# Performance work log

Hardware: AMD Instinct MI355X
Metric: run time of the kernel (lower is better)

## Reference

```python
import jax, jax.numpy as jnp
import numpy as np

EPS = 1e-8  # torch F.cosine_similarity eps


def setup_inputs() -> dict:
    key = jax.random.key(0)
    k1, k2, k3 = jax.random.split(key, 3)
    bn, cn, dim = 4096, 8192, 1024
    x = jax.random.normal(k1, (bn, dim), dtype=jnp.float32)
    positive = jax.random.normal(k2, (bn, dim), dtype=jnp.float32)
    negative = jax.random.normal(k3, (cn, dim), dtype=jnp.float32)
    return {"x": x, "positive": positive, "negative": negative}


def reference(x, positive, negative):
    bn = x.shape[0]
    nx = jnp.linalg.norm(x, axis=1)          # (bn,)
    npos = jnp.linalg.norm(positive, axis=1)  # (bn,)
    nneg = jnp.linalg.norm(negative, axis=1)  # (cn,)
    # positive cosine similarity, torch-style eps clamp on norm product
    sim = jnp.sum(x * positive, axis=1) / jnp.maximum(nx * npos, EPS)  # (bn,)
    # negative cosine similarities via one matmul instead of (bn,cn,dim) repeats
    neg_sim = (x @ negative.T) / jnp.maximum(nx[:, None] * nneg[None, :], EPS)  # (bn,cn)
    p = jnp.exp(sim) / jnp.sum(jnp.exp(neg_sim), axis=1)  # (bn,)
    loss = -jnp.sum(jnp.log(p)) / bn
    return loss
```

## Files before the change

### kernel.cpp

```cpp
#include <hip/hip_runtime.h>
#include <stdint.h>
#include <stddef.h>

#define DIM 1024
#define EPS 1e-8f

typedef __attribute__((ext_vector_type(4))) float f32x4;
typedef __attribute__((ext_vector_type(2))) long longx2;

__device__ __forceinline__ void async_copy16(const void* g, void* l) {
    __builtin_amdgcn_global_load_lds(
        (__attribute__((address_space(1))) void*)const_cast<void*>(g),
        (__attribute__((address_space(3))) void*)(l), 16, 0, 0);
}

#define PIPE_SYNC(N) asm volatile("s_waitcnt vmcnt(" #N ")\n\ts_barrier" ::: "memory")

__global__ __launch_bounds__(256)
void prep_all(const float* __restrict__ x, const float* __restrict__ pos,
              const float* __restrict__ neg,
              unsigned char* __restrict__ Xn, unsigned char* __restrict__ Nn,
              float* __restrict__ simOut, float* __restrict__ rowsum, int bn) {
    const int lane = threadIdx.x & 63;
    const int wave = threadIdx.x >> 6;
    const int grow = blockIdx.x * 4 + wave;
    const bool isX = grow < bn;
    const int row  = isX ? grow : grow - bn;
    const float* src = isX ? x : neg;
    unsigned char* dst = isX ? Xn : Nn;

    const float4* s = (const float4*)(src + (size_t)row * DIM);
    float4 xv[4], pv[4];
    float sxx = 0.f, spp = 0.f, sxp = 0.f;
#pragma unroll
    for (int i = 0; i < 4; i++) {
        xv[i] = s[lane + 64 * i];
        sxx += xv[i].x * xv[i].x + xv[i].y * xv[i].y + xv[i].z * xv[i].z + xv[i].w * xv[i].w;
    }
    if (isX) {
        const float4* p = (const float4*)(pos + (size_t)row * DIM);
#pragma unroll
        for (int i = 0; i < 4; i++) {
            pv[i] = p[lane + 64 * i];
            spp += pv[i].x * pv[i].x + pv[i].y * pv[i].y + pv[i].z * pv[i].z + pv[i].w * pv[i].w;
            sxp += xv[i].x * pv[i].x + xv[i].y * pv[i].y + xv[i].z * pv[i].z + xv[i].w * pv[i].w;
        }
#pragma unroll
        for (int off = 1; off < 64; off <<= 1) {
            sxx += __shfl_xor(sxx, off);
            spp += __shfl_xor(spp, off);
            sxp += __shfl_xor(sxp, off);
        }
    } else {
#pragma unroll
        for (int off = 1; off < 64; off <<= 1) sxx += __shfl_xor(sxx, off);
    }
    const float nx  = sqrtf(sxx);
    const float inv = (nx > 0.f) ? (16.f / nx) : 0.f;
    if (isX && lane == 0) {
        const float np = sqrtf(spp);
        simOut[row] = sxp / fmaxf(nx * np, EPS);
        rowsum[row] = 0.f;
    }
    unsigned int t;
    t = __builtin_amdgcn_cvt_pk_fp8_f32(xv[0].x * inv, xv[0].y * inv, 0, false);
    unsigned int q0 = __builtin_amdgcn_cvt_pk_fp8_f32(xv[0].z * inv, xv[0].w * inv, t, true);
    t = __builtin_amdgcn_cvt_pk_fp8_f32(xv[1].x * inv, xv[1].y * inv, 0, false);
    unsigned int q1 = __builtin_amdgcn_cvt_pk_fp8_f32(xv[1].z * inv, xv[1].w * inv, t, true);
    t = __builtin_amdgcn_cvt_pk_fp8_f32(xv[2].x * inv, xv[2].y * inv, 0, false);
    unsigned int q2 = __builtin_amdgcn_cvt_pk_fp8_f32(xv[2].z * inv, xv[2].w * inv, t, true);
    t = __builtin_amdgcn_cvt_pk_fp8_f32(xv[3].x * inv, xv[3].y * inv, 0, false);
    unsigned int q3 = __builtin_amdgcn_cvt_pk_fp8_f32(xv[3].z * inv, xv[3].w * inv, t, true);

    const int m  = lane & 3;
    const int d0 = (m & 1) * 32 + (m >> 1) * 8;
    unsigned char* wbase = dst + (size_t)row * DIM + (lane >> 2) * 64;
    *(unsigned long long*)(wbase + d0)      = ((unsigned long long)q1 << 32) | q0;
    *(unsigned long long*)(wbase + d0 + 16) = ((unsigned long long)q3 << 32) | q2;
}

__global__ __launch_bounds__(256)
void gemm_exp_rowsum(const unsigned char* __restrict__ Xn,
                     const unsigned char* __restrict__ Nn,
                     float* __restrict__ rowsum) {
    constexpr int KB   = DIM;
    constexpr int BK   = 64;
    constexpr int BUFB = 128 * BK;
    __shared__ __align__(16) unsigned char Ash[3][BUFB];
    __shared__ __align__(16) unsigned char Bsh[3][BUFB];

    const int tid  = threadIdx.x;
    const int lane = tid & 63;
    const int wave = tid >> 6;
    const int rowBase = blockIdx.y * 128;
    const int colBase = blockIdx.x * 128;

    const int srow   = lane >> 2;
    const int schunk = (lane & 3) ^ ((srow >> 1) & 3);
    const unsigned char* gA = Xn + (size_t)(rowBase + wave * 16 + srow) * KB + schunk * 16;
    const unsigned char* gB = Nn + (size_t)(colBase + wave * 16 + srow) * KB + schunk * 16;
    const int lgrp0 = (wave * 16) * BK;
    const int lgrp1 = (wave * 16 + 64) * BK;

    const f32x4 fz = {0.f, 0.f, 0.f, 0.f};
    f32x4 acc[4][4];
#pragma unroll
    for (int mi = 0; mi < 4; mi++)
#pragma unroll
        for (int ni = 0; ni < 4; ni++) acc[mi][ni] = fz;

    const int m0   = (wave >> 1) * 64;
    const int n0   = (wave & 1) * 64;
    const int quad = lane >> 4;
    const int mrow = lane & 15;
    const int kx   = (mrow >> 1) & 3;

    int aoff[4], boff[4];
#pragma unroll
    for (int i = 0; i < 4; i++) {
        aoff[i] = (m0 + i * 16 + mrow) * BK + ((quad ^ kx) << 4);
        boff[i] = (n0 + i * 16 + mrow) * BK + ((quad ^ kx) << 4);
    }

#define STAGE(buf, stg)                                                  \
    do {                                                                 \
        const int kq = (stg) * BK;                                       \
        async_copy16(gA + kq,            &Ash[buf][lgrp0]);              \
        async_copy16(gA + 64 * KB + kq,  &Ash[buf][lgrp1]);              \
        async_copy16(gB + kq,            &Bsh[buf][lgrp0]);              \
        async_copy16(gB + 64 * KB + kq,  &Bsh[buf][lgrp1]);              \
    } while (0)

#define COMPUTE(buf)                                                     \
    do {                                                                 \
        longx2 a2[4], b2[4];                                             \
        _Pragma("unroll")                                                \
        for (int i = 0; i < 4; i++) {                                    \
            a2[i] = *(const longx2*)&Ash[buf][aoff[i]];                  \
            b2[i] = *(const longx2*)&Bsh[buf][boff[i]];                  \
        }                                                                \
        _Pragma("unroll")                                                \
        for (int mi = 0; mi < 4; mi++)                                   \
            _Pragma("unroll")                                            \
            for (int ni = 0; ni < 4; ni++) {                             \
                acc[mi][ni] = __builtin_amdgcn_mfma_f32_16x16x32_fp8_fp8( \
                    a2[mi].x, b2[ni].x, acc[mi][ni], 0, 0, 0);           \
                acc[mi][ni] = __builtin_amdgcn_mfma_f32_16x16x32_fp8_fp8( \
                    a2[mi].y, b2[ni].y, acc[mi][ni], 0, 0, 0);           \
            }                                                            \
    } while (0)

    STAGE(0, 0);
    STAGE(1, 1);
    for (int it = 0; it < 4; it++) {
        const int s = 3 * it + 2;
        PIPE_SYNC(4); STAGE(2, s);     COMPUTE(0);
        PIPE_SYNC(4); STAGE(0, s + 1); COMPUTE(1);
        PIPE_SYNC(4); STAGE(1, s + 2); COMPUTE(2);
    }
    PIPE_SYNC(4); STAGE(2, 14); COMPUTE(0);
    PIPE_SYNC(4); STAGE(0, 15); COMPUTE(1);
    PIPE_SYNC(4);               COMPUTE(2);
    PIPE_SYNC(0);               COMPUTE(0);
#undef STAGE
#undef COMPUTE

#pragma unroll
    for (int mi = 0; mi < 4; mi++) {
        float rs0 = 0.f, rs1 = 0.f, rs2 = 0.f, rs3 = 0.f;
#pragma unroll
        for (int ni = 0; ni < 4; ni++) {
            rs0 += __expf(acc[mi][ni].x * 0.00390625f);
            rs1 += __expf(acc[mi][ni].y * 0.00390625f);
            rs2 += __expf(acc[mi][ni].z * 0.00390625f);
            rs3 += __expf(acc[mi][ni].w * 0.00390625f);
        }
#pragma unroll
        for (int off = 1; off < 16; off <<= 1) {
            rs0 += __shfl_xor(rs0, off);
            rs1 += __shfl_xor(rs1, off);
            rs2 += __shfl_xor(rs2, off);
            rs3 += __shfl_xor(rs3, off);
        }
        if ((lane & 15) == 0) {
            const int r = rowBase + m0 + mi * 16 + quad * 4;
            atomicAdd(&rowsum[r + 0], rs0);
            atomicAdd(&rowsum[r + 1], rs1);
            atomicAdd(&rowsum[r + 2], rs2);
            atomicAdd(&rowsum[r + 3], rs3);
        }
    }
}

__global__ __launch_bounds__(1024)
void loss_kernel(const float* __restrict__ rowsum, const float* __restrict__ sim,
                 float* __restrict__ out, int bn) {
    const int tid  = threadIdx.x;
    const int lane = tid & 63;
    const int wave = tid >> 6;
    float acc = 0.f;
    for (int i = tid; i < bn; i += 1024) acc += logf(rowsum[i]) - sim[i];
#pragma unroll
    for (int off = 1; off < 64; off <<= 1) acc += __shfl_xor(acc, off);
    __shared__ float red[16];
    if (lane == 0) red[wave] = acc;
    __syncthreads();
    if (tid == 0) {
        float t = 0.f;
#pragma unroll
        for (int i = 0; i < 16; i++) t += red[i];
        out[0] = t / (float)bn;
    }
}

extern "C" void kernel_launch(void* const* d_in, const int* in_sizes, int n_in,
                              void* d_out, int out_size, void* d_ws, size_t ws_size,
                              hipStream_t stream) {
    const float* x   = (const float*)d_in[0];
    const float* pos = (const float*)d_in[1];
    const float* neg = (const float*)d_in[2];
    const int bn = in_sizes[0] / DIM;
    const int cn = in_sizes[2] / DIM;

    unsigned char* Xn = (unsigned char*)d_ws;
    unsigned char* Nn = Xn + (size_t)bn * DIM;
    float* sim    = (float*)(Nn + (size_t)cn * DIM);
    float* rowsum = sim + bn;

    prep_all<<<dim3((bn + cn) / 4), dim3(256), 0, stream>>>(x, pos, neg, Xn, Nn, sim, rowsum, bn);
    gemm_exp_rowsum<<<dim3(cn / 128, bn / 128), dim3(256), 0, stream>>>(Xn, Nn, rowsum);
    loss_kernel<<<dim3(1), dim3(1024), 0, stream>>>(rowsum, sim, (float*)d_out, bn);
}
```

Measured before the change: 168.0 us.

## Switch GEMM to 32x32x64 scaled FP8 MFMA with folded descaling

Replaces the 16x16x32 FP8 MFMA pairs with the gfx950 scaled 32x32x64 f8f6f4 MFMA, using a block scale exponent to absorb the 1/256 normalization factor. The prep kernel's FP8 store layout becomes a simple lane-strided pattern to match the new operand fragment layout, and the epilogue reduction is reworked for 32-row accumulators. Launch bounds now request three blocks per CU. The aim is fewer, denser matrix instructions and fewer LDS reads per FLOP. The risk is that the fragment layout, swizzle and scale encoding must all match exactly, or the results are wrong.

```diff
diff --git a/kernel.cpp b/kernel.cpp
--- a/kernel.cpp
+++ b/kernel.cpp
@@ -5,8 +5,11 @@
 #define DIM 1024
 #define EPS 1e-8f
 
-typedef __attribute__((ext_vector_type(4))) float f32x4;
-typedef __attribute__((ext_vector_type(2))) long longx2;
+typedef __attribute__((ext_vector_type(4)))  int   i32x4;
+typedef __attribute__((ext_vector_type(8)))  int   i32x8;
+typedef __attribute__((ext_vector_type(16))) float f32x16;
+
+#define SCALE8 0x7B7B7B7B
 
 __device__ __forceinline__ void async_copy16(const void* g, void* l) {
     __builtin_amdgcn_global_load_lds(
@@ -72,14 +75,14 @@
     t = __builtin_amdgcn_cvt_pk_fp8_f32(xv[3].x * inv, xv[3].y * inv, 0, false);
     unsigned int q3 = __builtin_amdgcn_cvt_pk_fp8_f32(xv[3].z * inv, xv[3].w * inv, t, true);
 
-    const int m  = lane & 3;
-    const int d0 = (m & 1) * 32 + (m >> 1) * 8;
-    unsigned char* wbase = dst + (size_t)row * DIM + (lane >> 2) * 64;
-    *(unsigned long long*)(wbase + d0)      = ((unsigned long long)q1 << 32) | q0;
-    *(unsigned long long*)(wbase + d0 + 16) = ((unsigned long long)q3 << 32) | q2;
-}
-
-__global__ __launch_bounds__(256)
+    unsigned int* wr = (unsigned int*)(dst + (size_t)row * DIM);
+    wr[lane]       = q0;
+    wr[lane + 64]  = q1;
+    wr[lane + 128] = q2;
+    wr[lane + 192] = q3;
+}
+
+__global__ __launch_bounds__(256, 3)
 void gemm_exp_rowsum(const unsigned char* __restrict__ Xn,
                      const unsigned char* __restrict__ Nn,
                      float* __restrict__ rowsum) {
@@ -102,24 +105,27 @@
     const int lgrp0 = (wave * 16) * BK;
     const int lgrp1 = (wave * 16 + 64) * BK;
 
-    const f32x4 fz = {0.f, 0.f, 0.f, 0.f};
-    f32x4 acc[4][4];
-#pragma unroll
-    for (int mi = 0; mi < 4; mi++)
-#pragma unroll
-        for (int ni = 0; ni < 4; ni++) acc[mi][ni] = fz;
+    f32x16 acc[2][2];
+#pragma unroll
+    for (int mi = 0; mi < 2; mi++)
+#pragma unroll
+        for (int ni = 0; ni < 2; ni++)
+#pragma unroll
+            for (int e = 0; e < 16; e++) acc[mi][ni][e] = 0.f;
 
     const int m0   = (wave >> 1) * 64;
     const int n0   = (wave & 1) * 64;
-    const int quad = lane >> 4;
-    const int mrow = lane & 15;
+    const int mrow = lane & 31;
+    const int kh   = lane >> 5;
     const int kx   = (mrow >> 1) & 3;
-
-    int aoff[4], boff[4];
-#pragma unroll
-    for (int i = 0; i < 4; i++) {
-        aoff[i] = (m0 + i * 16 + mrow) * BK + ((quad ^ kx) << 4);
-        boff[i] = (n0 + i * 16 + mrow) * BK + ((quad ^ kx) << 4);
+    const int c0   = ((2 * kh + 0) ^ kx) << 4;
+    const int c1   = ((2 * kh + 1) ^ kx) << 4;
+
+    int arow[2], brow[2];
+#pragma unroll
+    for (int i = 0; i < 2; i++) {
+        arow[i] = (m0 + 32 * i + mrow) * BK;
+        brow[i] = (n0 + 32 * i + mrow) * BK;
     }
 
 #define STAGE(buf, stg)                                                  \
@@ -133,21 +139,22 @@
 
 #define COMPUTE(buf)                                                     \
     do {                                                                 \
-        longx2 a2[4], b2[4];                                             \
+        i32x8 Af[2], Bf[2];                                              \
         _Pragma("unroll")                                                \
-        for (int i = 0; i < 4; i++) {                                    \
-            a2[i] = *(const longx2*)&Ash[buf][aoff[i]];                  \
-            b2[i] = *(const longx2*)&Bsh[buf][boff[i]];                  \
+        for (int i = 0; i < 2; i++) {                                    \
+            i32x4 alo = *(const i32x4*)&Ash[buf][arow[i] + c0];          \
+            i32x4 ahi = *(const i32x4*)&Ash[buf][arow[i] + c1];          \
+            Af[i] = __builtin_shufflevector(alo, ahi, 0, 1, 2, 3, 4, 5, 6, 7); \
+            i32x4 blo = *(const i32x4*)&Bsh[buf][brow[i] + c0];          \
+            i32x4 bhi = *(const i32x4*)&Bsh[buf][brow[i] + c1];          \
+            Bf[i] = __builtin_shufflevector(blo, bhi, 0, 1, 2, 3, 4, 5, 6, 7); \
         }                                                                \
         _Pragma("unroll")                                                \
-        for (int mi = 0; mi < 4; mi++)                                   \
+        for (int mi = 0; mi < 2; mi++)                                   \
             _Pragma("unroll")                                            \
-            for (int ni = 0; ni < 4; ni++) {                             \
-                acc[mi][ni] = __builtin_amdgcn_mfma_f32_16x16x32_fp8_fp8( \
-                    a2[mi].x, b2[ni].x, acc[mi][ni], 0, 0, 0);           \
-                acc[mi][ni] = __builtin_amdgcn_mfma_f32_16x16x32_fp8_fp8( \
-                    a2[mi].y, b2[ni].y, acc[mi][ni], 0, 0, 0);           \
-            }                                                            \
+            for (int ni = 0; ni < 2; ni++)                               \
+                acc[mi][ni] = __builtin_amdgcn_mfma_scale_f32_32x32x64_f8f6f4( \
+                    Af[mi], Bf[ni], acc[mi][ni], 0, 0, 0, SCALE8, 0, SCALE8); \
     } while (0)
 
     STAGE(0, 0);
@@ -166,28 +173,23 @@
 #undef COMPUTE
 
 #pragma unroll
-    for (int mi = 0; mi < 4; mi++) {
-        float rs0 = 0.f, rs1 = 0.f, rs2 = 0.f, rs3 = 0.f;
-#pragma unroll
-        for (int ni = 0; ni < 4; ni++) {
-            rs0 += __expf(acc[mi][ni].x * 0.00390625f);
-            rs1 += __expf(acc[mi][ni].y * 0.00390625f);
-            rs2 += __expf(acc[mi][ni].z * 0.00390625f);
-            rs3 += __expf(acc[mi][ni].w * 0.00390625f);
-        }
-#pragma unroll
-        for (int off = 1; off < 16; off <<= 1) {
-            rs0 += __shfl_xor(rs0, off);
-            rs1 += __shfl_xor(rs1, off);
-            rs2 += __shfl_xor(rs2, off);
-            rs3 += __shfl_xor(rs3, off);
-        }
-        if ((lane & 15) == 0) {
-            const int r = rowBase + m0 + mi * 16 + quad * 4;
-            atomicAdd(&rowsum[r + 0], rs0);
-            atomicAdd(&rowsum[r + 1], rs1);
-            atomicAdd(&rowsum[r + 2], rs2);
-            atomicAdd(&rowsum[r + 3], rs3);
+    for (int mi = 0; mi < 2; mi++) {
+        float rs[16];
+#pragma unroll
+        for (int r = 0; r < 16; r++) {
+            float v = __expf(acc[mi][0][r]) + __expf(acc[mi][1][r]);
+            v += __shfl_xor(v, 1);
+            v += __shfl_xor(v, 2);
+            v += __shfl_xor(v, 4);
+            v += __shfl_xor(v, 8);
+            v += __shfl_xor(v, 16);
+            rs[r] = v;
+        }
+        if ((lane & 31) == 0) {
+            const int rbase = rowBase + m0 + 32 * mi + 4 * kh;
+#pragma unroll
+            for (int r = 0; r < 16; r++)
+                atomicAdd(&rowsum[rbase + (r & 3) + 8 * (r >> 2)], rs[r]);
         }
     }
 }
```

After: 218.6 us. 1.3x slower.

## Switch GEMM to scaled 16x16x128 FP8 MFMA with single-buffer BK=128 tiles

Applied to the files above, without the earlier changes.

Replaces the 16x16x32 fp8 MFMA pair with the gfx950 scaled 16x16x128 f8f6f4 MFMA. The folded scale exponent (0x7B, i.e. 2^-4 per operand) removes the post-GEMM 1/256 multiply. The K tile grows to 128 with a new XOR swizzle and plain linear fp8 writes in prep, so each wave issues fewer, wider MFMAs. The triple-buffered pipeline is dropped for a single buffer with a full wait and barrier every stage, which exposes load latency. Launch bounds now ask for 3 blocks per CU so occupancy can hide that latency instead.

```diff
diff --git a/kernel.cpp b/kernel.cpp
--- a/kernel.cpp
+++ b/kernel.cpp
@@ -5,16 +5,17 @@
 #define DIM 1024
 #define EPS 1e-8f
 
-typedef __attribute__((ext_vector_type(4))) float f32x4;
-typedef __attribute__((ext_vector_type(2))) long longx2;
+typedef __attribute__((ext_vector_type(4)))  int   i32x4;
+typedef __attribute__((ext_vector_type(8)))  int   i32x8;
+typedef __attribute__((ext_vector_type(4)))  float f32x4;
+
+#define SCALE8 0x7B7B7B7B
 
 __device__ __forceinline__ void async_copy16(const void* g, void* l) {
     __builtin_amdgcn_global_load_lds(
         (__attribute__((address_space(1))) void*)const_cast<void*>(g),
         (__attribute__((address_space(3))) void*)(l), 16, 0, 0);
 }
-
-#define PIPE_SYNC(N) asm volatile("s_waitcnt vmcnt(" #N ")\n\ts_barrier" ::: "memory")
 
 __global__ __launch_bounds__(256)
 void prep_all(const float* __restrict__ x, const float* __restrict__ pos,
@@ -72,22 +73,21 @@
     t = __builtin_amdgcn_cvt_pk_fp8_f32(xv[3].x * inv, xv[3].y * inv, 0, false);
     unsigned int q3 = __builtin_amdgcn_cvt_pk_fp8_f32(xv[3].z * inv, xv[3].w * inv, t, true);
 
-    const int m  = lane & 3;
-    const int d0 = (m & 1) * 32 + (m >> 1) * 8;
-    unsigned char* wbase = dst + (size_t)row * DIM + (lane >> 2) * 64;
-    *(unsigned long long*)(wbase + d0)      = ((unsigned long long)q1 << 32) | q0;
-    *(unsigned long long*)(wbase + d0 + 16) = ((unsigned long long)q3 << 32) | q2;
-}
-
-__global__ __launch_bounds__(256)
+    unsigned int* wr = (unsigned int*)(dst + (size_t)row * DIM);
+    wr[lane]       = q0;
+    wr[lane + 64]  = q1;
+    wr[lane + 128] = q2;
+    wr[lane + 192] = q3;
+}
+
+__global__ __launch_bounds__(256, 3)
 void gemm_exp_rowsum(const unsigned char* __restrict__ Xn,
                      const unsigned char* __restrict__ Nn,
                      float* __restrict__ rowsum) {
-    constexpr int KB   = DIM;
-    constexpr int BK   = 64;
-    constexpr int BUFB = 128 * BK;
-    __shared__ __align__(16) unsigned char Ash[3][BUFB];
-    __shared__ __align__(16) unsigned char Bsh[3][BUFB];
+    constexpr int KB = DIM;
+    constexpr int BK = 128;
+    __shared__ __align__(16) unsigned char Ash[128 * BK];
+    __shared__ __align__(16) unsigned char Bsh[128 * BK];
 
     const int tid  = threadIdx.x;
     const int lane = tid & 63;
@@ -95,12 +95,11 @@
     const int rowBase = blockIdx.y * 128;
     const int colBase = blockIdx.x * 128;
 
-    const int srow   = lane >> 2;
-    const int schunk = (lane & 3) ^ ((srow >> 1) & 3);
-    const unsigned char* gA = Xn + (size_t)(rowBase + wave * 16 + srow) * KB + schunk * 16;
-    const unsigned char* gB = Nn + (size_t)(colBase + wave * 16 + srow) * KB + schunk * 16;
-    const int lgrp0 = (wave * 16) * BK;
-    const int lgrp1 = (wave * 16 + 64) * BK;
+    const int srow = lane >> 3;
+    const int sch  = (lane & 7) ^ srow;
+    const int w32  = wave * 32;
+    const unsigned char* gA = Xn + (size_t)(rowBase + w32 + srow) * KB + sch * 16;
+    const unsigned char* gB = Nn + (size_t)(colBase + w32 + srow) * KB + sch * 16;
 
     const f32x4 fz = {0.f, 0.f, 0.f, 0.f};
     f32x4 acc[4][4];
@@ -111,57 +110,54 @@
 
     const int m0   = (wave >> 1) * 64;
     const int n0   = (wave & 1) * 64;
-    const int quad = lane >> 4;
     const int mrow = lane & 15;
-    const int kx   = (mrow >> 1) & 3;
+    const int q    = lane >> 4;
+    const int c0   = ((2 * q) ^ (mrow & 7)) << 4;
 
     int aoff[4], boff[4];
 #pragma unroll
     for (int i = 0; i < 4; i++) {
-        aoff[i] = (m0 + i * 16 + mrow) * BK + ((quad ^ kx) << 4);
-        boff[i] = (n0 + i * 16 + mrow) * BK + ((quad ^ kx) << 4);
-    }
-
-#define STAGE(buf, stg)                                                  \
-    do {                                                                 \
-        const int kq = (stg) * BK;                                       \
-        async_copy16(gA + kq,            &Ash[buf][lgrp0]);              \
-        async_copy16(gA + 64 * KB + kq,  &Ash[buf][lgrp1]);              \
-        async_copy16(gB + kq,            &Bsh[buf][lgrp0]);              \
-        async_copy16(gB + 64 * KB + kq,  &Bsh[buf][lgrp1]);              \
+        aoff[i] = (m0 + 16 * i + mrow) * BK + c0;
+        boff[i] = (n0 + 16 * i + mrow) * BK + c0;
+    }
+
+#define STAGE(stg)                                                        \
+    do {                                                                  \
+        const int kq = (stg) * BK;                                        \
+        _Pragma("unroll")                                                 \
+        for (int i = 0; i < 4; i++) {                                     \
+            async_copy16(gA + (size_t)(8 * i) * KB + kq, Ash + (w32 + 8 * i) * BK); \
+            async_copy16(gB + (size_t)(8 * i) * KB + kq, Bsh + (w32 + 8 * i) * BK); \
+        }                                                                 \
     } while (0)
 
-#define COMPUTE(buf)                                                     \
-    do {                                                                 \
-        longx2 a2[4], b2[4];                                             \
-        _Pragma("unroll")                                                \
-        for (int i = 0; i < 4; i++) {                                    \
-            a2[i] = *(const longx2*)&Ash[buf][aoff[i]];                  \
-            b2[i] = *(const longx2*)&Bsh[buf][boff[i]];                  \
-        }                                                                \
-        _Pragma("unroll")                                                \
-        for (int mi = 0; mi < 4; mi++)                                   \
-            _Pragma("unroll")                                            \
-            for (int ni = 0; ni < 4; ni++) {                             \
-                acc[mi][ni] = __builtin_amdgcn_mfma_f32_16x16x32_fp8_fp8( \
-                    a2[mi].x, b2[ni].x, acc[mi][ni], 0, 0, 0);           \
-                acc[mi][ni] = __builtin_amdgcn_mfma_f32_16x16x32_fp8_fp8( \
-                    a2[mi].y, b2[ni].y, acc[mi][ni], 0, 0, 0);           \
-            }                                                            \
+#define COMPUTE()                                                         \
+    do {                                                                  \
+        i32x8 Af[4], Bf[4];                                               \
+        _Pragma("unroll")                                                 \
+        for (int i = 0; i < 4; i++) {                                     \
+            i32x4 alo = *(const i32x4*)(Ash + aoff[i]);                   \
+            i32x4 ahi = *(const i32x4*)(Ash + (aoff[i] ^ 16));            \
+            Af[i] = __builtin_shufflevector(alo, ahi, 0, 1, 2, 3, 4, 5, 6, 7); \
+            i32x4 blo = *(const i32x4*)(Bsh + boff[i]);                   \
+            i32x4 bhi = *(const i32x4*)(Bsh + (boff[i] ^ 16));            \
+            Bf[i] = __builtin_shufflevector(blo, bhi, 0, 1, 2, 3, 4, 5, 6, 7); \
+        }                                                                 \
+        _Pragma("unroll")                                                 \
+        for (int mi = 0; mi < 4; mi++)                                    \
+            _Pragma("unroll")                                             \
+            for (int ni = 0; ni < 4; ni++)                                \
+                acc[mi][ni] = __builtin_amdgcn_mfma_scale_f32_16x16x128_f8f6f4( \
+                    Af[mi], Bf[ni], acc[mi][ni], 0, 0, 0, SCALE8, 0, SCALE8); \
     } while (0)
 
-    STAGE(0, 0);
-    STAGE(1, 1);
-    for (int it = 0; it < 4; it++) {
-        const int s = 3 * it + 2;
-        PIPE_SYNC(4); STAGE(2, s);     COMPUTE(0);
-        PIPE_SYNC(4); STAGE(0, s + 1); COMPUTE(1);
-        PIPE_SYNC(4); STAGE(1, s + 2); COMPUTE(2);
-    }
-    PIPE_SYNC(4); STAGE(2, 14); COMPUTE(0);
-    PIPE_SYNC(4); STAGE(0, 15); COMPUTE(1);
-    PIPE_SYNC(4);               COMPUTE(2);
-    PIPE_SYNC(0);               COMPUTE(0);
+#pragma unroll
+    for (int s = 0; s < 8; s++) {
+        STAGE(s);
+        asm volatile("s_waitcnt vmcnt(0)\n\ts_barrier" ::: "memory");
+        COMPUTE();
+        __syncthreads();
+    }
 #undef STAGE
 #undef COMPUTE
 
@@ -170,10 +166,10 @@
         float rs0 = 0.f, rs1 = 0.f, rs2 = 0.f, rs3 = 0.f;
 #pragma unroll
         for (int ni = 0; ni < 4; ni++) {
-            rs0 += __expf(acc[mi][ni].x * 0.00390625f);
-            rs1 += __expf(acc[mi][ni].y * 0.00390625f);
-            rs2 += __expf(acc[mi][ni].z * 0.00390625f);
-            rs3 += __expf(acc[mi][ni].w * 0.00390625f);
+            rs0 += __expf(acc[mi][ni].x);
+            rs1 += __expf(acc[mi][ni].y);
+            rs2 += __expf(acc[mi][ni].z);
+            rs3 += __expf(acc[mi][ni].w);
         }
 #pragma unroll
         for (int off = 1; off < 16; off <<= 1) {
@@ -183,7 +179,7 @@
             rs3 += __shfl_xor(rs3, off);
         }
         if ((lane & 15) == 0) {
-            const int r = rowBase + m0 + mi * 16 + quad * 4;
+            const int r = rowBase + m0 + mi * 16 + q * 4;
             atomicAdd(&rowsum[r + 0], rs0);
             atomicAdd(&rowsum[r + 1], rs1);
             atomicAdd(&rowsum[r + 2], rs2);
```

Result: no change. 169.2 us (+0.7%).
